# Kernel tuning notes

Measured on AMD Instinct MI355X. Metric: run time of the kernel, lower is better.

## Reference

```python
import jax, jax.numpy as jnp
import numpy as np

N, E = 50000, 800000
IN, HID, OUT, H = 128, 64, 64, 2
NC, EC = 5, 2  # node / edge num classes
NUM_ITER, GAMMA = 2, 1.0


def gat_conv(x, src, dst, eattr, W, att_s, att_d, We, att_e, b, n_nodes):
    """PyG GATConv with concat=False, edge_dim, add_self_loops(fill='mean')."""
    Hh, C = att_s.shape
    # self loops; loop edge_attr = per-dst-node mean of incident edge features
    ones_e = jnp.ones((src.shape[0],), x.dtype)
    deg = jax.ops.segment_sum(ones_e, dst, num_segments=n_nodes)
    loop_attr = jax.ops.segment_sum(eattr, dst, num_segments=n_nodes) / jnp.maximum(deg, 1.0)[:, None]
    loop = jnp.arange(n_nodes)
    src = jnp.concatenate([src, loop])
    dst = jnp.concatenate([dst, loop])
    eattr = jnp.concatenate([eattr, loop_attr], axis=0)
    h = (x @ W).reshape(n_nodes, Hh, C)            # [N,H,C]
    e = (eattr @ We).reshape(-1, Hh, C)            # [E',H,C]
    a_s = jnp.einsum('nhc,hc->nh', h, att_s)
    a_d = jnp.einsum('nhc,hc->nh', h, att_d)
    a_e = jnp.einsum('ehc,hc->eh', e, att_e)
    a = jax.nn.leaky_relu(a_s[src] + a_d[dst] + a_e, 0.2)  # [E',H]
    amax = jax.ops.segment_max(a, dst, num_segments=n_nodes)
    ea = jnp.exp(a - amax[dst])
    denom = jax.ops.segment_sum(ea, dst, num_segments=n_nodes)
    alpha = ea / (denom[dst] + 1e-16)
    out = jax.ops.segment_sum(alpha[:, :, None] * h[src], dst, num_segments=n_nodes)
    return out.mean(axis=1) + b                     # concat=False -> head mean


def factor_graph(node_logits, edge_logits, src, dst, node_fw, edge_fw):
    n = node_logits.shape[0]
    p_n = jax.nn.softmax(node_logits, axis=-1)
    p_e = jax.nn.softmax(edge_logits, axis=-1)
    ones_e = jnp.ones((src.shape[0],), node_logits.dtype)
    deg = jax.ops.segment_sum(ones_e, src, num_segments=n) + jax.ops.segment_sum(ones_e, dst, num_segments=n)
    avg_ef = edge_fw[1:, 1:].mean()
    avg_nf = node_fw[1:, 1:].mean()
    for _ in range(NUM_ITER):
        nab = 1.0 - p_n[:, 0]
        ena = jnp.maximum(nab[src], nab[dst])                       # [E]
        new_ab = p_e[:, 1:] * (1.0 + GAMMA * ena[:, None] * avg_ef)
        p_e = jnp.concatenate([p_e[:, :1], new_ab], axis=-1)
        p_e = p_e / p_e.sum(axis=-1, keepdims=True)
        eab = 1.0 - p_e[:, 0]
        s = jax.ops.segment_sum(eab, src, num_segments=n) + jax.ops.segment_sum(eab, dst, num_segments=n)
        mean = s / (deg + 1e-6)
        new_nab = p_n[:, 1:] * (1.0 + GAMMA * mean[:, None] * avg_nf)
        p_n = jnp.concatenate([p_n[:, :1], new_nab], axis=-1)
        p_n = p_n / p_n.sum(axis=-1, keepdims=True)
    return jnp.log(p_n + 1e-9), jnp.log(p_e + 1e-9)


def setup_inputs() -> dict:
    key = jax.random.key(0)
    ks = jax.random.split(key, 24)
    s = 0.1
    d = dict(
        x=jax.random.normal(ks[0], (N, IN), jnp.float32),
        edge_index=jax.random.randint(ks[1], (2, E), 0, N),
        edge_attr=jax.random.normal(ks[2], (E, 2), jnp.float32),
        W1=jax.random.normal(ks[3], (IN, H * HID), jnp.float32) * s,
        att_src1=jax.random.normal(ks[4], (H, HID), jnp.float32) * s,
        att_dst1=jax.random.normal(ks[5], (H, HID), jnp.float32) * s,
        We1=jax.random.normal(ks[6], (2, H * HID), jnp.float32) * s,
        att_e1=jax.random.normal(ks[7], (H, HID), jnp.float32) * s,
        b1=jnp.zeros((HID,), jnp.float32),
        W2=jax.random.normal(ks[8], (HID, H * OUT), jnp.float32) * s,
        att_src2=jax.random.normal(ks[9], (H, OUT), jnp.float32) * s,
        att_dst2=jax.random.normal(ks[10], (H, OUT), jnp.float32) * s,
        We2=jax.random.normal(ks[11], (2, H * OUT), jnp.float32) * s,
        att_e2=jax.random.normal(ks[12], (H, OUT), jnp.float32) * s,
        b2=jnp.zeros((OUT,), jnp.float32),
        Wn=jax.random.normal(ks[13], (OUT, NC), jnp.float32) * s,
        bn=jnp.zeros((NC,), jnp.float32),
        Wec=jax.random.normal(ks[14], (OUT, EC), jnp.float32) * s,
        bec=jnp.zeros((EC,), jnp.float32),
        node_fw=jnp.ones((NC, EC), jnp.float32),
        edge_fw=jnp.ones((EC, NC), jnp.float32),
    )
    return d


def reference(x, edge_index, edge_attr, W1, att_src1, att_dst1, We1, att_e1, b1,
              W2, att_src2, att_dst2, We2, att_e2, b2, Wn, bn, Wec, bec,
              node_fw, edge_fw):
    src, dst = edge_index[0], edge_index[1]
    h = gat_conv(x, src, dst, edge_attr, W1, att_src1, att_dst1, We1, att_e1, b1, N)
    h = jax.nn.relu(h)
    h = gat_conv(h, src, dst, edge_attr, W2, att_src2, att_dst2, We2, att_e2, b2, N)
    node_logits = h @ Wn + bn                       # [N,NC]
    edge_emb = (h[src] + h[dst]) * 0.5              # [E,OUT]
    edge_logits = edge_emb @ Wec + bec              # [E,EC]
    return factor_graph(node_logits, edge_logits, src, dst, node_fw, edge_fw)
```

## Files before the change

### kernel.cpp

```cpp
#include <hip/hip_runtime.h>
#include <math.h>


static inline int cdiv_i(long long a, long long b) { return (int)((a + b - 1) / b); }

#define BSH 8
#define CBK 8

typedef __attribute__((ext_vector_type(8))) short bf16x8s;
typedef __attribute__((ext_vector_type(4))) float f32x4;

__device__ __forceinline__ float fexp(float x) {
  return __builtin_amdgcn_exp2f(x * 1.44269504088896f);
}
__device__ __forceinline__ float flog(float x) {
  return __builtin_amdgcn_logf(x) * 0.693147180559945f;
}
__device__ __forceinline__ float frcp(float x) {
  return __builtin_amdgcn_rcpf(x);
}

__device__ __forceinline__ unsigned short bf16r(float x) {
  unsigned u = __float_as_uint(x);
  return (unsigned short)((u + 0x7fffu + ((u >> 16) & 1u)) >> 16);
}
__device__ __forceinline__ unsigned pack_bf2(float a, float b) {
  unsigned ua = __float_as_uint(a), ub = __float_as_uint(b);
  unsigned ra = (ua + 0x7fffu + ((ua >> 16) & 1u)) >> 16;
  unsigned rb = (ub + 0x7fffu + ((ub >> 16) & 1u)) & 0xffff0000u;
  return ra | rb;
}
__device__ __forceinline__ float bf_lo(unsigned v) { return __uint_as_float(v << 16); }
__device__ __forceinline__ float bf_hi(unsigned v) { return __uint_as_float(v & 0xffff0000u); }

__device__ __forceinline__ float dot64_f4(const float* __restrict__ a,
                                          const float* __restrict__ b) {
  float s = 0.f;
#pragma unroll
  for (int c = 0; c < 64; c += 4) {
    float4 av = *(const float4*)&a[c];
    float4 bv = *(const float4*)&b[c];
    s += av.x * bv.x + av.y * bv.y + av.z * bv.z + av.w * bv.w;
  }
  return s;
}

__global__ __launch_bounds__(256)
void k_prep(const float* __restrict__ W1, const float* __restrict__ as1,
            const float* __restrict__ ad1, const float* __restrict__ atte1,
            const float* __restrict__ We1,
            const float* __restrict__ W2, const float* __restrict__ as2,
            const float* __restrict__ ad2, const float* __restrict__ atte2,
            const float* __restrict__ We2,
            const float* __restrict__ node_fw, const float* __restrict__ edge_fw,
            const float* __restrict__ bec, float* __restrict__ consts,
            unsigned short* __restrict__ wf1, unsigned short* __restrict__ wf2,
            int* __restrict__ cur_d, int* __restrict__ cur_s) {
  __shared__ float wext1[128 * 4], wext2[64 * 4];
  int t = threadIdx.x;
  for (int o = t; o < 192 * 4; o += 256) {
    bool l1 = o < 512;
    int oo = l1 ? o : o - 512;
    int k = oo >> 2, j = oo & 3;
    const float* att = l1 ? ((j < 2 ? as1 : ad1) + (j & 1) * 64)
                          : ((j < 2 ? as2 : ad2) + (j & 1) * 64);
    const float* wr = l1 ? (W1 + k * 128 + (j & 1) * 64)
                         : (W2 + k * 128 + (j & 1) * 64);
    float s = dot64_f4(wr, att);
    if (l1) wext1[oo] = s; else wext2[oo] = s;
  }
  if (blockIdx.x == 0) {
    cur_d[t] = 0; cur_s[t] = 0;
    if (t < 8) {
      int layer = t >> 2, h = (t >> 1) & 1, k = t & 1;
      const float* We = layer ? We2 : We1;
      const float* ae = layer ? atte2 : atte1;
      consts[layer * 4 + h * 2 + k] = dot64_f4(&We[k * 128 + h * 64], &ae[h * 64]);
    } else if (t == 8) {
      float ef = 0.f;
      for (int j = 1; j < 5; ++j) ef += edge_fw[5 + j];
      consts[8] = ef * 0.25f;
    } else if (t == 9) {
      float nf = 0.f;
      for (int i = 1; i < 5; ++i) nf += node_fw[i * 2 + 1];
      consts[9] = nf * 0.25f;
    } else if (t == 10) {
      consts[10] = bec[1] - bec[0];
    }
  }
  __syncthreads();
  const int tot1 = 4 * 9 * 512, tot2 = 2 * 9 * 512;
  for (int o = blockIdx.x * 256 + t; o < tot1; o += gridDim.x * 256) {
    int kc = o / (9 * 512), rem = o % (9 * 512);
    int ct = rem / 512, li = rem % 512;
    int lane = li >> 3, j = li & 7;
    int k = kc * 32 + ((lane >> 4) << 3) + j, c = lane & 15;
    float v = (ct < 8) ? W1[k * 128 + ct * 16 + c] : (c < 4 ? wext1[k * 4 + c] : 0.f);
    wf1[o] = bf16r(v);
  }
  for (int o = blockIdx.x * 256 + t; o < tot2; o += gridDim.x * 256) {
    int kc = o / (9 * 512), rem = o % (9 * 512);
    int ct = rem / 512, li = rem % 512;
    int lane = li >> 3, j = li & 7;
    int k = kc * 32 + ((lane >> 4) << 3) + j, c = lane & 15;
    float v = (ct < 8) ? W2[k * 128 + ct * 16 + c] : (c < 4 ? wext2[k * 4 + c] : 0.f);
    wf2[o] = bf16r(v);
  }
}

__global__ void k_bkt_hist(const int* __restrict__ src, const int* __restrict__ dst,
                           int* __restrict__ hist_d, int* __restrict__ hist_s,
                           int nbkt, int E) {
  __shared__ int hd[256], hs[256];
  int t = threadIdx.x;
  hd[t] = 0; hs[t] = 0;
  __syncthreads();
  for (int e = blockIdx.x * blockDim.x + t; e < E; e += gridDim.x * blockDim.x) {
    atomicAdd(&hd[dst[e] >> BSH], 1);
    atomicAdd(&hs[src[e] >> BSH], 1);
  }
  __syncthreads();
  if (t < nbkt) {
    if (hd[t]) atomicAdd(&hist_d[t], hd[t]);
    if (hs[t]) atomicAdd(&hist_s[t], hs[t]);
  }
}

__global__ void k_bkt_scan(int* __restrict__ cur_d, int* __restrict__ base_d,
                           int* __restrict__ cur_s, int* __restrict__ base_s, int nbkt) {
  __shared__ int l[256];
  int t = threadIdx.x;
  int v = (t < nbkt) ? cur_d[t] : 0;
  l[t] = v; __syncthreads();
  for (int off = 1; off < 256; off <<= 1) {
    int x = (t >= off) ? l[t - off] : 0; __syncthreads();
    l[t] += x; __syncthreads();
  }
  int incl = l[t];
  if (t < nbkt) { base_d[t] = incl - v; cur_d[t] = incl - v; }
  if (t == nbkt - 1) base_d[nbkt] = incl;
  __syncthreads();
  v = (t < nbkt) ? cur_s[t] : 0;
  l[t] = v; __syncthreads();
  for (int off = 1; off < 256; off <<= 1) {
    int x = (t >= off) ? l[t - off] : 0; __syncthreads();
    l[t] += x; __syncthreads();
  }
  incl = l[t];
  if (t < nbkt) { base_s[t] = incl - v; cur_s[t] = incl - v; }
  if (t == nbkt - 1) base_s[nbkt] = incl;
}

__global__ __launch_bounds__(256)
void k_bkt_scatter(const int* __restrict__ src, const int* __restrict__ dst,
                   const float* __restrict__ eattr2,
                   int* __restrict__ cur_d, int* __restrict__ cur_s,
                   int4* __restrict__ stage_d, int2* __restrict__ stage_s,
                   int nbkt, int E) {
  __shared__ int cd[256], cs[256], bd[256], bs[256];
  int t = threadIdx.x;
  cd[t] = 0; cs[t] = 0;
  __syncthreads();
  int base = blockIdx.x * 256 * CBK;
  int s[CBK], d[CBK]; unsigned ep[CBK];
#pragma unroll
  for (int c = 0; c < CBK; ++c) {
    int e = base + c * 256 + t;
    if (e < E) {
      s[c] = src[e]; d[c] = dst[e];
      float2 ev = *(const float2*)&eattr2[2 * e];
      ep[c] = pack_bf2(ev.x, ev.y);
      atomicAdd(&cd[d[c] >> BSH], 1);
      atomicAdd(&cs[s[c] >> BSH], 1);
    } else s[c] = -1;
  }
  __syncthreads();
  if (t < nbkt) {
    bd[t] = cd[t] ? atomicAdd(&cur_d[t], cd[t]) : 0;
    bs[t] = cs[t] ? atomicAdd(&cur_s[t], cs[t]) : 0;
    cd[t] = 0; cs[t] = 0;
  }
  __syncthreads();
#pragma unroll
  for (int c = 0; c < CBK; ++c) {
    if (s[c] < 0) continue;
    int db = d[c] >> BSH, sb = s[c] >> BSH;
    int pos = bd[db] + atomicAdd(&cd[db], 1);
    stage_d[pos] = make_int4(s[c], d[c], (int)ep[c], 0);
    int pos2 = bs[sb] + atomicAdd(&cs[sb], 1);
    stage_s[pos2] = make_int2(s[c], d[c]);
  }
}

__global__ __launch_bounds__(256)
void k_bkt_sort(const int4* __restrict__ stage_d, const int* __restrict__ base_d,
                int* __restrict__ rowptr_d, int2* __restrict__ rec,
                int* __restrict__ dstnbr,
                const int2* __restrict__ stage_s, const int* __restrict__ base_s,
                int* __restrict__ rowptr_s, int* __restrict__ srcnbr,
                int N, int nbkt) {
  int t = threadIdx.x;
  __shared__ int cnt[256], cur[256], l[256];
  if ((int)blockIdx.x < nbkt) {
    int b = blockIdx.x;
    int nlo = b << BSH;
    int b0 = base_d[b], b1 = base_d[b + 1];
    cnt[t] = 0;
    __syncthreads();
    for (int j = b0 + t; j < b1; j += 256)
      atomicAdd(&cnt[stage_d[j].y - nlo], 1);
    __syncthreads();
    int v = cnt[t];
    l[t] = v; __syncthreads();
    for (int off = 1; off < 256; off <<= 1) {
      int x = (t >= off) ? l[t - off] : 0; __syncthreads();
      l[t] += x; __syncthreads();
    }
    int excl = l[t] - v;
    if (nlo + t < N) rowptr_d[nlo + t] = b0 + excl;
    cur[t] = excl;
    __syncthreads();
    for (int j = b0 + t; j < b1; j += 256) {
      int4 r = stage_d[j];
      int pos = b0 + atomicAdd(&cur[r.y - nlo], 1);
      rec[pos] = make_int2(r.x, r.z);
      dstnbr[pos] = r.x;
    }
  } else {
    int b = blockIdx.x - nbkt;
    int nlo = b << BSH;
    int b0 = base_s[b], b1 = base_s[b + 1];
    cnt[t] = 0;
    __syncthreads();
    for (int j = b0 + t; j < b1; j += 256)
      atomicAdd(&cnt[stage_s[j].x - nlo], 1);
    __syncthreads();
    int v = cnt[t];
    l[t] = v; __syncthreads();
    for (int off = 1; off < 256; off <<= 1) {
      int x = (t >= off) ? l[t - off] : 0; __syncthreads();
      l[t] += x; __syncthreads();
    }
    int excl = l[t] - v;
    if (nlo + t < N) rowptr_s[nlo + t] = b0 + excl;
    cur[t] = excl;
    __syncthreads();
    for (int j = b0 + t; j < b1; j += 256) {
      int2 r = stage_s[j];
      int pos = b0 + atomicAdd(&cur[r.x - nlo], 1);
      srcnbr[pos] = r.y;
    }
  }
}

template<int K>
__global__ __launch_bounds__(256)
void k_gemm_att_mfma(const float* __restrict__ A, const unsigned short* __restrict__ Wf,
                     unsigned* __restrict__ h16, float* __restrict__ asd, int N) {
  int wv = threadIdx.x >> 6, lane = threadIdx.x & 63;
  int r0 = blockIdx.x * 64 + wv * 16;
  int arow = r0 + (lane & 15);
  int kbase = (lane >> 4) * 8;
  f32x4 acc[9];
#pragma unroll
  for (int ct = 0; ct < 9; ++ct) acc[ct] = (f32x4){0.f, 0.f, 0.f, 0.f};

#pragma unroll
  for (int kc = 0; kc < K; kc += 32) {
    float4 v0 = make_float4(0.f, 0.f, 0.f, 0.f);
    float4 v1 = make_float4(0.f, 0.f, 0.f, 0.f);
    if (arow < N) {
      const float* ap = A + (long long)arow * K + kc + kbase;
      v0 = *(const float4*)ap;
      v1 = *(const float4*)(ap + 4);
    }
    bf16x8s a;
    a[0] = (short)bf16r(v0.x); a[1] = (short)bf16r(v0.y);
    a[2] = (short)bf16r(v0.z); a[3] = (short)bf16r(v0.w);
    a[4] = (short)bf16r(v1.x); a[5] = (short)bf16r(v1.y);
    a[6] = (short)bf16r(v1.z); a[7] = (short)bf16r(v1.w);
    const unsigned short* wp = Wf + (size_t)(kc >> 5) * 9 * 512 + lane * 8;
#pragma unroll
    for (int ct = 0; ct < 9; ++ct) {
      bf16x8s b = *(const bf16x8s*)(wp + ct * 512);
      acc[ct] = __builtin_amdgcn_mfma_f32_16x16x32_bf16(a, b, acc[ct], 0, 0, 0);
    }
  }
  int c = lane & 15;
  int orow = r0 + (lane >> 4) * 4;
#pragma unroll
  for (int r = 0; r < 4; ++r) {
    int gr = orow + r;
    if (gr >= N) continue;
#pragma unroll
    for (int ct = 0; ct < 4; ++ct)
      h16[((long long)gr << 6) | (ct * 16 + c)] = pack_bf2(acc[ct][r], acc[ct + 4][r]);
    if (c < 4) asd[gr * 4 + c] = acc[8][r];
  }
}

template<bool RELU, bool HEAD>
__global__ __launch_bounds__(256)
void k_gat_pull(const int* __restrict__ rowptr, const int2* __restrict__ rec,
                const float* __restrict__ asd, const unsigned* __restrict__ h16,
                const float* __restrict__ we, const float* __restrict__ bias,
                const float* __restrict__ Wn, const float* __restrict__ bn,
                const float* __restrict__ Wec,
                float* __restrict__ out, float* __restrict__ p_n,
                int2* __restrict__ fgn8, int N, int E) {
  __shared__ int2 ed[4][64];
  int wv = threadIdx.x >> 6, lane = threadIdx.x & 63;
  int g = lane >> 4;
  int tl = lane & 15;
  int d = blockIdx.x * 16 + wv * 4 + g;
  if (d >= N) return;
  int r0 = rowptr[d];
  int r1 = (d + 1 < N) ? rowptr[d + 1] : E;
  int deg = r1 - r0;
  float4 Ad = *(const float4*)&asd[4 * d];
  float w0 = we[0], w1 = we[1], w2 = we[2], w3 = we[3];
  float den0 = 0.f, den1 = 0.f, se0 = 0.f, se1 = 0.f;
  float accA[4] = {0.f, 0.f, 0.f, 0.f}, accB[4] = {0.f, 0.f, 0.f, 0.f};
  int2* edg = &ed[wv][g << 4];
  for (int cb = 0; cb < deg; cb += 16) {
    int j = cb + tl;
    int s = 0; unsigned eapk = 0;
    if (j < deg) {
      int2 rc = rec[r0 + j];
      s = rc.x;
      unsigned ep = (unsigned)rc.y;
      float e0 = bf_lo(ep), e1 = bf_hi(ep);
      float4 As = *(const float4*)&asd[4 * s];
      float x0 = As.x + Ad.z + e0 * w0 + e1 * w1;
      float x1 = As.y + Ad.w + e0 * w2 + e1 * w3;
      x0 = x0 >= 0.f ? x0 : 0.2f * x0;
      x1 = x1 >= 0.f ? x1 : 0.2f * x1;
      float ea0 = fexp(x0), ea1 = fexp(x1);
      eapk = pack_bf2(ea0, ea1);
      den0 += ea0; den1 += ea1; se0 += e0; se1 += e1;
    }
    edg[tl] = make_int2(s, (int)eapk);
    int m = min(16, deg - cb);
    int j2 = 0;
    for (; j2 + 2 <= m; j2 += 2) {
      int2 va = edg[j2];
      int2 vb = edg[j2 + 1];
      uint4 qa = *(const uint4*)&h16[((long long)va.x << 6) | (tl << 2)];
      uint4 qb = *(const uint4*)&h16[((long long)vb.x << 6) | (tl << 2)];
      float a0 = bf_lo((unsigned)va.y), a1 = bf_hi((unsigned)va.y);
      float b0 = bf_lo((unsigned)vb.y), b1 = bf_hi((unsigned)vb.y);
      accA[0] += a0 * bf_lo(qa.x); accB[0] += a1 * bf_hi(qa.x);
      accA[1] += a0 * bf_lo(qa.y); accB[1] += a1 * bf_hi(qa.y);
      accA[2] += a0 * bf_lo(qa.z); accB[2] += a1 * bf_hi(qa.z);
      accA[3] += a0 * bf_lo(qa.w); accB[3] += a1 * bf_hi(qa.w);
      accA[0] += b0 * bf_lo(qb.x); accB[0] += b1 * bf_hi(qb.x);
      accA[1] += b0 * bf_lo(qb.y); accB[1] += b1 * bf_hi(qb.y);
      accA[2] += b0 * bf_lo(qb.z); accB[2] += b1 * bf_hi(qb.z);
      accA[3] += b0 * bf_lo(qb.w); accB[3] += b1 * bf_hi(qb.w);
    }
    if (j2 < m) {
      int2 va = edg[j2];
      uint4 qa = *(const uint4*)&h16[((long long)va.x << 6) | (tl << 2)];
      float a0 = bf_lo((unsigned)va.y), a1 = bf_hi((unsigned)va.y);
      accA[0] += a0 * bf_lo(qa.x); accB[0] += a1 * bf_hi(qa.x);
      accA[1] += a0 * bf_lo(qa.y); accB[1] += a1 * bf_hi(qa.y);
      accA[2] += a0 * bf_lo(qa.z); accB[2] += a1 * bf_hi(qa.z);
      accA[3] += a0 * bf_lo(qa.w); accB[3] += a1 * bf_hi(qa.w);
    }
  }
  for (int off = 8; off; off >>= 1) {
    den0 += __shfl_xor(den0, off); den1 += __shfl_xor(den1, off);
    se0  += __shfl_xor(se0, off);  se1  += __shfl_xor(se1, off);
  }
  float id = frcp(fmaxf((float)deg, 1.0f));
  float le0 = se0 * id, le1 = se1 * id;
  float x0 = Ad.x + Ad.z + le0 * w0 + le1 * w1;
  float x1 = Ad.y + Ad.w + le0 * w2 + le1 * w3;
  x0 = x0 >= 0.f ? x0 : 0.2f * x0;
  x1 = x1 >= 0.f ? x1 : 0.2f * x1;
  float eas0 = fexp(x0), eas1 = fexp(x1);
  den0 += eas0; den1 += eas1;
  uint4 qd = *(const uint4*)&h16[((long long)d << 6) | (tl << 2)];
  accA[0] += eas0 * bf_lo(qd.x); accB[0] += eas1 * bf_hi(qd.x);
  accA[1] += eas0 * bf_lo(qd.y); accB[1] += eas1 * bf_hi(qd.y);
  accA[2] += eas0 * bf_lo(qd.z); accB[2] += eas1 * bf_hi(qd.z);
  accA[3] += eas0 * bf_lo(qd.w); accB[3] += eas1 * bf_hi(qd.w);
  float rcp0 = frcp(den0 + 1e-16f), rcp1 = frcp(den1 + 1e-16f);
  float4 bs = *(const float4*)&bias[tl << 2];
  float v0 = 0.5f * (accA[0] * rcp0 + accB[0] * rcp1) + bs.x;
  float v1 = 0.5f * (accA[1] * rcp0 + accB[1] * rcp1) + bs.y;
  float v2 = 0.5f * (accA[2] * rcp0 + accB[2] * rcp1) + bs.z;
  float v3 = 0.5f * (accA[3] * rcp0 + accB[3] * rcp1) + bs.w;
  if (HEAD) {
    int c0 = tl << 2;
    float pv[7];
#pragma unroll
    for (int j = 0; j < 5; ++j)
      pv[j] = v0 * Wn[c0 * 5 + j] + v1 * Wn[(c0 + 1) * 5 + j]
            + v2 * Wn[(c0 + 2) * 5 + j] + v3 * Wn[(c0 + 3) * 5 + j];
    pv[5] = v0 * Wec[c0 * 2] + v1 * Wec[(c0 + 1) * 2]
          + v2 * Wec[(c0 + 2) * 2] + v3 * Wec[(c0 + 3) * 2];
    pv[6] = v0 * Wec[c0 * 2 + 1] + v1 * Wec[(c0 + 1) * 2 + 1]
          + v2 * Wec[(c0 + 2) * 2 + 1] + v3 * Wec[(c0 + 3) * 2 + 1];
    for (int off = 8; off; off >>= 1) {
#pragma unroll
      for (int j = 0; j < 7; ++j) pv[j] += __shfl_xor(pv[j], off);
    }
    if (tl == 0) {
      float l[5]; float m = -1e30f;
#pragma unroll
      for (int j = 0; j < 5; ++j) { l[j] = pv[j] + bn[j]; m = fmaxf(m, l[j]); }
      float ssum = 0.f;
#pragma unroll
      for (int j = 0; j < 5; ++j) { l[j] = fexp(l[j] - m); ssum += l[j]; }
      float inv = frcp(ssum);
#pragma unroll
      for (int j = 0; j < 5; ++j) p_n[5 * d + j] = l[j] * inv;
      float nab0 = (ssum - l[0]) * inv;
      fgn8[d] = make_int2(__float_as_int(pv[6] - pv[5]), (int)pack_bf2(nab0, 0.f));
    }
  } else {
    if (RELU) {
      v0 = fmaxf(v0, 0.f); v1 = fmaxf(v1, 0.f);
      v2 = fmaxf(v2, 0.f); v3 = fmaxf(v3, 0.f);
    }
    *(float4*)&out[(long long)d * 64 + (tl << 2)] = make_float4(v0, v1, v2, v3);
  }
}

__device__ __forceinline__ float fg_eab(float t, float c) {
  return c * frcp(c + fexp(-t));
}

__global__ void k_fg_pull1(const int* __restrict__ rowptr_d, const int* __restrict__ dstnbr,
                           const int* __restrict__ rowptr_s, const int* __restrict__ srcnbr,
                           float* __restrict__ p_n, int2* __restrict__ fgn8,
                           const float* __restrict__ consts, int N, int E) {
  int gid = blockIdx.x * blockDim.x + threadIdx.x;
  int n = gid >> 2, q = gid & 3;
  if (n >= N) return;
  int2 F = fgn8[n];
  float qv = __uint_as_float((unsigned)F.x);
  float nab0 = bf_lo((unsigned)F.y);
  float avg_ef = consts[8], avg_nf = consts[9], dbec = consts[10];
  int rd0 = rowptr_d[n], rd1 = (n + 1 < N) ? rowptr_d[n + 1] : E;
  int rs0 = rowptr_s[n], rs1 = (n + 1 < N) ? rowptr_s[n + 1] : E;
  float s_eab = 0.f;
  for (int j = rd0 + q; j < rd1; j += 4) {
    int2 Fo = fgn8[dstnbr[j]];
    float t = 0.5f * (qv + __uint_as_float((unsigned)Fo.x)) + dbec;
    float c = 1.0f + fmaxf(nab0, bf_lo((unsigned)Fo.y)) * avg_ef;
    s_eab += fg_eab(t, c);
  }
  for (int j = rs0 + q; j < rs1; j += 4) {
    int2 Fo = fgn8[srcnbr[j]];
    float t = 0.5f * (qv + __uint_as_float((unsigned)Fo.x)) + dbec;
    float c = 1.0f + fmaxf(nab0, bf_lo((unsigned)Fo.y)) * avg_ef;
    s_eab += fg_eab(t, c);
  }
  s_eab += __shfl_xor(s_eab, 1);
  s_eab += __shfl_xor(s_eab, 2);
  if (q) return;
  float deg = (float)((rd1 - rd0) + (rs1 - rs0));
  float mean = s_eab * frcp(deg + 1e-6f);
  float f = 1.0f + mean * avg_nf;
  float p0 = p_n[5 * n], p1 = p_n[5 * n + 1], p2 = p_n[5 * n + 2],
        p3 = p_n[5 * n + 3], p4 = p_n[5 * n + 4];
  float rest = (p1 + p2 + p3 + p4) * f;
  float inv = frcp(p0 + rest);
  p_n[5 * n]     = p0 * inv;
  p_n[5 * n + 1] = p1 * f * inv;
  p_n[5 * n + 2] = p2 * f * inv;
  p_n[5 * n + 3] = p3 * f * inv;
  p_n[5 * n + 4] = p4 * f * inv;
  fgn8[n].y = (int)pack_bf2(nab0, rest * inv);
}

__global__ void k_fg_final(const int* __restrict__ rowptr_d, const int* __restrict__ dstnbr,
                           const int* __restrict__ rowptr_s, const int* __restrict__ srcnbr,
                           const float* __restrict__ p_n, const int2* __restrict__ fgn8,
                           const float* __restrict__ consts,
                           const int* __restrict__ src, const int* __restrict__ dst,
                           float* __restrict__ out_n, float* __restrict__ out_e,
                           int N, int E, int nodeBlocks) {
  float avg_ef = consts[8], dbec = consts[10];
  if ((int)blockIdx.x < nodeBlocks) {
    int gid = blockIdx.x * blockDim.x + threadIdx.x;
    int n = gid >> 2, q = gid & 3;
    if (n >= N) return;
    float avg_nf = consts[9];
    int2 F = fgn8[n];
    float qv = __uint_as_float((unsigned)F.x);
    float nab0 = bf_lo((unsigned)F.y), nab1 = bf_hi((unsigned)F.y);
    int rd0 = rowptr_d[n], rd1 = (n + 1 < N) ? rowptr_d[n + 1] : E;
    int rs0 = rowptr_s[n], rs1 = (n + 1 < N) ? rowptr_s[n + 1] : E;
    float s_eab = 0.f;
    for (int j = rd0 + q; j < rd1; j += 4) {
      int2 Fo = fgn8[dstnbr[j]];
      float t = 0.5f * (qv + __uint_as_float((unsigned)Fo.x)) + dbec;
      float c = (1.0f + fmaxf(nab0, bf_lo((unsigned)Fo.y)) * avg_ef)
              * (1.0f + fmaxf(nab1, bf_hi((unsigned)Fo.y)) * avg_ef);
      s_eab += fg_eab(t, c);
    }
    for (int j = rs0 + q; j < rs1; j += 4) {
      int2 Fo = fgn8[srcnbr[j]];
      float t = 0.5f * (qv + __uint_as_float((unsigned)Fo.x)) + dbec;
      float c = (1.0f + fmaxf(nab0, bf_lo((unsigned)Fo.y)) * avg_ef)
              * (1.0f + fmaxf(nab1, bf_hi((unsigned)Fo.y)) * avg_ef);
      s_eab += fg_eab(t, c);
    }
    s_eab += __shfl_xor(s_eab, 1);
    s_eab += __shfl_xor(s_eab, 2);
    if (q) return;
    float deg = (float)((rd1 - rd0) + (rs1 - rs0));
    float mean = s_eab * frcp(deg + 1e-6f);
    float f = 1.0f + mean * avg_nf;
    float p0 = p_n[5 * n], p1 = p_n[5 * n + 1], p2 = p_n[5 * n + 2],
          p3 = p_n[5 * n + 3], p4 = p_n[5 * n + 4];
    float rest = (p1 + p2 + p3 + p4) * f;
    float inv = frcp(p0 + rest);
    out_n[5 * n]     = flog(p0 * inv + 1e-9f);
    out_n[5 * n + 1] = flog(p1 * f * inv + 1e-9f);
    out_n[5 * n + 2] = flog(p2 * f * inv + 1e-9f);
    out_n[5 * n + 3] = flog(p3 * f * inv + 1e-9f);
    out_n[5 * n + 4] = flog(p4 * f * inv + 1e-9f);
  } else {
    int e0 = ((blockIdx.x - nodeBlocks) * blockDim.x + threadIdx.x) * 2;
    if (e0 >= E) return;
    int ne = min(2, E - e0);
    int sv[2], dv[2];
#pragma unroll
    for (int u = 0; u < 2; ++u) {
      sv[u] = (u < ne) ? src[e0 + u] : 0;
      dv[u] = (u < ne) ? dst[e0 + u] : 0;
    }
    int2 Fs[2], Fd[2];
#pragma unroll
    for (int u = 0; u < 2; ++u) { Fs[u] = fgn8[sv[u]]; Fd[u] = fgn8[dv[u]]; }
#pragma unroll
    for (int u = 0; u < 2; ++u) {
      if (u >= ne) break;
      float t = 0.5f * (__uint_as_float((unsigned)Fs[u].x) +
                        __uint_as_float((unsigned)Fd[u].x)) + dbec;
      float c = (1.0f + fmaxf(bf_lo((unsigned)Fs[u].y), bf_lo((unsigned)Fd[u].y)) * avg_ef)
              * (1.0f + fmaxf(bf_hi((unsigned)Fs[u].y), bf_hi((unsigned)Fd[u].y)) * avg_ef);
      float ei = fexp(-t);
      float r = frcp(c + ei);
      float pe1 = c * r, pe0 = ei * r;
      *(float2*)&out_e[2 * (e0 + u)] = make_float2(flog(pe0 + 1e-9f), flog(pe1 + 1e-9f));
    }
  }
}

extern "C" void kernel_launch(void* const* d_in, const int* in_sizes, int n_in,
                              void* d_out, int out_size, void* d_ws, size_t ws_size,
                              hipStream_t stream) {
  const float* x      = (const float*)d_in[0];
  const int*   ei     = (const int*)d_in[1];
  const float* eattr  = (const float*)d_in[2];
  const float* W1     = (const float*)d_in[3];
  const float* atts1  = (const float*)d_in[4];
  const float* attd1  = (const float*)d_in[5];
  const float* We1    = (const float*)d_in[6];
  const float* atte1  = (const float*)d_in[7];
  const float* b1     = (const float*)d_in[8];
  const float* W2     = (const float*)d_in[9];
  const float* atts2  = (const float*)d_in[10];
  const float* attd2  = (const float*)d_in[11];
  const float* We2    = (const float*)d_in[12];
  const float* atte2  = (const float*)d_in[13];
  const float* b2     = (const float*)d_in[14];
  const float* Wn     = (const float*)d_in[15];
  const float* bn     = (const float*)d_in[16];
  const float* Wec    = (const float*)d_in[17];
  const float* bec    = (const float*)d_in[18];
  const float* nodefw = (const float*)d_in[19];
  const float* edgefw = (const float*)d_in[20];

  const int N = in_sizes[0] / 128;
  const int E = in_sizes[1] / 2;
  const int* src = ei;
  const int* dst = ei + E;
  const int nbkt = (N + 255) >> BSH;

  float* out_n = (float*)d_out;
  float* out_e = out_n + (long long)N * 5;

  size_t off = 0;
  float* base = (float*)d_ws;
  auto carve = [&](size_t nelem) { float* p = base + off; off += (nelem + 3) & ~(size_t)3; return p; };
  unsigned* h16      = (unsigned*)carve((size_t)N * 64);
  float*    x2       = carve((size_t)N * 64);
  float*    asd      = carve((size_t)N * 4);
  int2*     rec      = (int2*)carve((size_t)E * 2);
  int*      srcnbr   = (int*)carve((size_t)E);
  int*      dstnbr   = (int*)carve((size_t)E);
  int*      rowptr_d = (int*)carve((size_t)N);
  int*      rowptr_s = (int*)carve((size_t)N);
  int*      bktcur_d = (int*)carve(256);
  int*      bktcur_s = (int*)carve(256);
  int*      bktbas_d = (int*)carve(260);
  int*      bktbas_s = (int*)carve(260);
  float*    p_n      = carve((size_t)N * 5);
  int2*     fgn8     = (int2*)carve((size_t)N * 2);
  float*    consts   = carve(16);
  unsigned short* wf1 = (unsigned short*)carve(9216);
  unsigned short* wf2 = (unsigned short*)carve(4608);
  if (off * sizeof(float) > ws_size) return;

  int4* stage_d = (int4*)h16;
  int2* stage_s = (int2*)x2;

  const int B = 256;
  const int gE2 = cdiv_i((long long)E, B * 2);
  const int gN4 = cdiv_i((long long)N * 4, B);

  k_prep<<<24, 256, 0, stream>>>(W1, atts1, attd1, atte1, We1,
                                 W2, atts2, attd2, atte2, We2,
                                 nodefw, edgefw, bec, consts, wf1, wf2,
                                 bktcur_d, bktcur_s);
  k_bkt_hist<<<256, 256, 0, stream>>>(src, dst, bktcur_d, bktcur_s, nbkt, E);
  k_bkt_scan<<<1, 256, 0, stream>>>(bktcur_d, bktbas_d, bktcur_s, bktbas_s, nbkt);
  k_bkt_scatter<<<cdiv_i(E, 256 * CBK), 256, 0, stream>>>(src, dst, eattr, bktcur_d, bktcur_s,
                                                          stage_d, stage_s, nbkt, E);
  k_bkt_sort<<<2 * nbkt, 256, 0, stream>>>(stage_d, bktbas_d, rowptr_d, rec, dstnbr,
                                           stage_s, bktbas_s, rowptr_s, srcnbr, N, nbkt);

  k_gemm_att_mfma<128><<<cdiv_i(N, 64), 256, 0, stream>>>(x, wf1, h16, asd, N);
  k_gat_pull<true, false><<<cdiv_i(N, 16), 256, 0, stream>>>(
      rowptr_d, rec, asd, h16, consts, b1,
      nullptr, nullptr, nullptr, x2, nullptr, nullptr, N, E);

  k_gemm_att_mfma<64><<<cdiv_i(N, 64), 256, 0, stream>>>(x2, wf2, h16, asd, N);
  k_gat_pull<false, true><<<cdiv_i(N, 16), 256, 0, stream>>>(
      rowptr_d, rec, asd, h16, consts + 4, b2,
      Wn, bn, Wec, nullptr, p_n, fgn8, N, E);

  k_fg_pull1<<<gN4, B, 0, stream>>>(rowptr_d, dstnbr, rowptr_s, srcnbr,
                                    p_n, fgn8, consts, N, E);
  k_fg_final<<<gN4 + gE2, B, 0, stream>>>(rowptr_d, dstnbr, rowptr_s, srcnbr,
                                          p_n, fgn8, consts, src, dst,
                                          out_n, out_e, N, E, gN4);
}
```

Before: 196.8 us.

## Sort destination nodes by in-degree to balance GAT pull workloads

Builds an in-degree histogram while sorting buckets, scans it, and scatters node ids into a degree-sorted permutation. Both GAT pull kernels then visit nodes in that order, so the 16-lane groups within a wavefront handle nodes of similar degree and spend less time diverged in the edge loop. The cost is two extra small kernel launches, an indirection through perm, and poorer locality when writing outputs and reading asd/rowptr by destination. With random graphs the degrees vary little (mean 16), which limits the gain.

```diff
diff --git a/kernel.cpp b/kernel.cpp
--- a/kernel.cpp
+++ b/kernel.cpp
@@ -55,7 +55,8 @@
             const float* __restrict__ node_fw, const float* __restrict__ edge_fw,
             const float* __restrict__ bec, float* __restrict__ consts,
             unsigned short* __restrict__ wf1, unsigned short* __restrict__ wf2,
-            int* __restrict__ cur_d, int* __restrict__ cur_s) {
+            int* __restrict__ cur_d, int* __restrict__ cur_s,
+            int* __restrict__ dbin) {
   __shared__ float wext1[128 * 4], wext2[64 * 4];
   int t = threadIdx.x;
   for (int o = t; o < 192 * 4; o += 256) {
@@ -70,7 +71,7 @@
     if (l1) wext1[oo] = s; else wext2[oo] = s;
   }
   if (blockIdx.x == 0) {
-    cur_d[t] = 0; cur_s[t] = 0;
+    cur_d[t] = 0; cur_s[t] = 0; dbin[t] = 0;
     if (t < 8) {
       int layer = t >> 2, h = (t >> 1) & 1, k = t & 1;
       const float* We = layer ? We2 : We1;
@@ -195,7 +196,7 @@
 __global__ __launch_bounds__(256)
 void k_bkt_sort(const int4* __restrict__ stage_d, const int* __restrict__ base_d,
                 int* __restrict__ rowptr_d, int2* __restrict__ rec,
-                int* __restrict__ dstnbr,
+                int* __restrict__ dstnbr, int* __restrict__ dbin,
                 const int2* __restrict__ stage_s, const int* __restrict__ base_s,
                 int* __restrict__ rowptr_s, int* __restrict__ srcnbr,
                 int N, int nbkt) {
@@ -211,6 +212,7 @@
       atomicAdd(&cnt[stage_d[j].y - nlo], 1);
     __syncthreads();
     int v = cnt[t];
+    if (nlo + t < N) atomicAdd(&dbin[min(v, 255)], 1);
     l[t] = v; __syncthreads();
     for (int off = 1; off < 256; off <<= 1) {
       int x = (t >= off) ? l[t - off] : 0; __syncthreads();
@@ -253,6 +255,42 @@
   }
 }
 
+__global__ void k_deg_scan(int* __restrict__ dbin) {
+  __shared__ int l[256];
+  int t = threadIdx.x;
+  int v = dbin[t];
+  l[t] = v; __syncthreads();
+  for (int off = 1; off < 256; off <<= 1) {
+    int x = (t >= off) ? l[t - off] : 0; __syncthreads();
+    l[t] += x; __syncthreads();
+  }
+  dbin[t] = l[t] - v;
+}
+
+__global__ __launch_bounds__(256)
+void k_deg_scatter(const int* __restrict__ rowptr_d, int* __restrict__ dcur,
+                   int* __restrict__ perm, int N, int E) {
+  __shared__ int cnt[256], base_[256];
+  int t = threadIdx.x;
+  int n = blockIdx.x * 256 + t;
+  cnt[t] = 0;
+  __syncthreads();
+  int bin = -1;
+  if (n < N) {
+    int deg = ((n + 1 < N) ? rowptr_d[n + 1] : E) - rowptr_d[n];
+    bin = min(deg, 255);
+    atomicAdd(&cnt[bin], 1);
+  }
+  __syncthreads();
+  base_[t] = cnt[t] ? atomicAdd(&dcur[t], cnt[t]) : 0;
+  cnt[t] = 0;
+  __syncthreads();
+  if (n < N) {
+    int pos = base_[bin] + atomicAdd(&cnt[bin], 1);
+    perm[pos] = n;
+  }
+}
+
 template<int K>
 __global__ __launch_bounds__(256)
 void k_gemm_att_mfma(const float* __restrict__ A, const unsigned short* __restrict__ Wf,
@@ -301,7 +339,8 @@
 
 template<bool RELU, bool HEAD>
 __global__ __launch_bounds__(256)
-void k_gat_pull(const int* __restrict__ rowptr, const int2* __restrict__ rec,
+void k_gat_pull(const int* __restrict__ perm,
+                const int* __restrict__ rowptr, const int2* __restrict__ rec,
                 const float* __restrict__ asd, const unsigned* __restrict__ h16,
                 const float* __restrict__ we, const float* __restrict__ bias,
                 const float* __restrict__ Wn, const float* __restrict__ bn,
@@ -312,8 +351,9 @@
   int wv = threadIdx.x >> 6, lane = threadIdx.x & 63;
   int g = lane >> 4;
   int tl = lane & 15;
-  int d = blockIdx.x * 16 + wv * 4 + g;
-  if (d >= N) return;
+  int pidx = blockIdx.x * 16 + wv * 4 + g;
+  if (pidx >= N) return;
+  int d = perm[pidx];
   int r0 = rowptr[d];
   int r1 = (d + 1 < N) ? rowptr[d + 1] : E;
   int deg = r1 - r0;
@@ -597,10 +637,12 @@
   int*      dstnbr   = (int*)carve((size_t)E);
   int*      rowptr_d = (int*)carve((size_t)N);
   int*      rowptr_s = (int*)carve((size_t)N);
+  int*      perm     = (int*)carve((size_t)N);
   int*      bktcur_d = (int*)carve(256);
   int*      bktcur_s = (int*)carve(256);
   int*      bktbas_d = (int*)carve(260);
   int*      bktbas_s = (int*)carve(260);
+  int*      dbin     = (int*)carve(256);
   float*    p_n      = carve((size_t)N * 5);
   int2*     fgn8     = (int2*)carve((size_t)N * 2);
   float*    consts   = carve(16);
@@ -614,26 +656,29 @@
   const int B = 256;
   const int gE2 = cdiv_i((long long)E, B * 2);
   const int gN4 = cdiv_i((long long)N * 4, B);
+  const int gN1 = cdiv_i(N, B);
 
   k_prep<<<24, 256, 0, stream>>>(W1, atts1, attd1, atte1, We1,
                                  W2, atts2, attd2, atte2, We2,
                                  nodefw, edgefw, bec, consts, wf1, wf2,
-                                 bktcur_d, bktcur_s);
+                                 bktcur_d, bktcur_s, dbin);
   k_bkt_hist<<<256, 256, 0, stream>>>(src, dst, bktcur_d, bktcur_s, nbkt, E);
   k_bkt_scan<<<1, 256, 0, stream>>>(bktcur_d, bktbas_d, bktcur_s, bktbas_s, nbkt);
   k_bkt_scatter<<<cdiv_i(E, 256 * CBK), 256, 0, stream>>>(src, dst, eattr, bktcur_d, bktcur_s,
                                                           stage_d, stage_s, nbkt, E);
-  k_bkt_sort<<<2 * nbkt, 256, 0, stream>>>(stage_d, bktbas_d, rowptr_d, rec, dstnbr,
+  k_bkt_sort<<<2 * nbkt, 256, 0, stream>>>(stage_d, bktbas_d, rowptr_d, rec, dstnbr, dbin,
                                            stage_s, bktbas_s, rowptr_s, srcnbr, N, nbkt);
+  k_deg_scan<<<1, 256, 0, stream>>>(dbin);
+  k_deg_scatter<<<gN1, 256, 0, stream>>>(rowptr_d, dbin, perm, N, E);
 
   k_gemm_att_mfma<128><<<cdiv_i(N, 64), 256, 0, stream>>>(x, wf1, h16, asd, N);
   k_gat_pull<true, false><<<cdiv_i(N, 16), 256, 0, stream>>>(
-      rowptr_d, rec, asd, h16, consts, b1,
+      perm, rowptr_d, rec, asd, h16, consts, b1,
       nullptr, nullptr, nullptr, x2, nullptr, nullptr, N, E);
 
   k_gemm_att_mfma<64><<<cdiv_i(N, 64), 256, 0, stream>>>(x2, wf2, h16, asd, N);
   k_gat_pull<false, true><<<cdiv_i(N, 16), 256, 0, stream>>>(
-      rowptr_d, rec, asd, h16, consts + 4, b2,
+      perm, rowptr_d, rec, asd, h16, consts + 4, b2,
       Wn, bn, Wec, nullptr, p_n, fgn8, N, E);
 
   k_fg_pull1<<<gN4, B, 0, stream>>>(rowptr_d, dstnbr, rowptr_s, srcnbr,
```

New measurement: 344.9 us. 75.2% more time.
